# Performance work log

Hardware: AMD Instinct MI355X
Metric: run time of the kernel (lower is better)

The kernel has to match this reference:

```python
import jax, jax.numpy as jnp
import numpy as np
from jax import lax

B, T, L = 32, 64, 1500        # flows, max packets per flow, packet length (MTU)
H, DC = 128, 100              # lstm hidden, cnn feature dim
KS, ST = 5, 3                 # conv kernel/stride
FLAT = 54 * 32                # conv output length 1500->499->165->54, 32 channels


def setup_inputs() -> dict:
    key = jax.random.key(0)
    ks = jax.random.split(key, 12)
    s = 0.05
    X = jax.random.normal(ks[0], (B, T, L), jnp.float32)
    lengths = jax.random.randint(ks[1], (B,), 1, T + 1, dtype=jnp.int32)
    conv1_w = jax.random.normal(ks[2], (128, 1, KS), jnp.float32) * s
    conv2_w = jax.random.normal(ks[3], (32, 128, KS), jnp.float32) * s
    conv3_w = jax.random.normal(ks[4], (32, 32, KS), jnp.float32) * s
    lin_w = jax.random.normal(ks[5], (DC, FLAT), jnp.float32) * s
    w_ih0 = jax.random.normal(ks[6], (4 * H, DC), jnp.float32) * s
    w_hh0 = jax.random.normal(ks[7], (4 * H, H), jnp.float32) * s
    w_ih1 = jax.random.normal(ks[8], (4 * H, H), jnp.float32) * s
    w_hh1 = jax.random.normal(ks[9], (4 * H, H), jnp.float32) * s
    fc1_w = jax.random.normal(ks[10], (10, H), jnp.float32) * s
    fc2_w = jax.random.normal(ks[11], (2, 10), jnp.float32) * s
    return {"X": X, "lengths": lengths, "conv1_w": conv1_w, "conv2_w": conv2_w,
            "conv3_w": conv3_w, "lin_w": lin_w, "w_ih0": w_ih0, "w_hh0": w_hh0,
            "w_ih1": w_ih1, "w_hh1": w_hh1, "fc1_w": fc1_w, "fc2_w": fc2_w}


def _conv(x, w):
    # x: [N, Cin, L], w: [Cout, Cin, K] -> valid conv, stride 3 (torch Conv1d semantics)
    return lax.conv_general_dilated(x, w, (ST,), 'VALID',
                                    dimension_numbers=('NCH', 'OIH', 'NCH'))


def _lstm_layer(xs, mask, w_ih, w_hh):
    # xs: [T, B, D]; mask: [T, B] (True = valid step); no biases (bias=False)
    Bn = xs.shape[1]
    h0 = jnp.zeros((Bn, H), xs.dtype)
    c0 = jnp.zeros((Bn, H), xs.dtype)

    def step(carry, inp):
        h, c = carry
        x_t, m_t = inp
        gates = x_t @ w_ih.T + h @ w_hh.T          # [B, 4H]
        i, f, g, o = jnp.split(gates, 4, axis=-1)  # torch gate order i,f,g,o
        i, f, o = jax.nn.sigmoid(i), jax.nn.sigmoid(f), jax.nn.sigmoid(o)
        g = jnp.tanh(g)
        c_new = f * c + i * g
        h_new = o * jnp.tanh(c_new)
        m = m_t[:, None]
        h = jnp.where(m, h_new, h)  # freeze state past each flow's length
        c = jnp.where(m, c_new, c)
        return (h, c), h

    (h_f, c_f), hs = lax.scan(step, (h0, c0), (xs, mask))
    return hs, h_f


def reference(X, lengths, conv1_w, conv2_w, conv3_w, lin_w,
              w_ih0, w_hh0, w_ih1, w_hh1, fc1_w, fc2_w):
    leaky = jax.nn.leaky_relu  # slope 0.01 matches torch default
    # ODCNN over every packet (batched over all B*T packets instead of python loops)
    x = X.reshape(B * T, 1, L)
    x = leaky(_conv(x, conv1_w))   # [BT, 128, 499]
    x = leaky(_conv(x, conv2_w))   # [BT, 32, 165]
    x = leaky(_conv(x, conv3_w))   # [BT, 32, 54]
    feats = x.reshape(B * T, FLAT) @ lin_w.T          # [BT, 100] (no activation)
    feats = feats.reshape(B, T, DC).transpose(1, 0, 2)  # [T, B, 100]
    mask = jnp.arange(T)[:, None] < lengths[None, :]     # [T, B]
    hs1, _ = _lstm_layer(feats, mask, w_ih0, w_hh0)
    _, h2 = _lstm_layer(hs1, mask, w_ih1, w_hh1)         # h at step len-1, top layer
    out = leaky(h2 @ fc1_w.T)
    out = leaky(out @ fc2_w.T)                           # [B, out_dim]
    return out
```

## Files before the change

kernel.cpp:

```cpp
#include <hip/hip_runtime.h>
#include <hip/hip_bf16.h>

#define B_ 32
#define T_ 64
#define H_ 128
#define L3OUT 54
#define FLAT_ 1728

typedef __attribute__((ext_vector_type(8))) short bf16x8;
typedef __attribute__((ext_vector_type(4))) float f32x4;

__device__ __forceinline__ float leakyf(float v) { return v > 0.f ? v : 0.01f * v; }
__device__ __forceinline__ float sigmoidf_(float v) { return 1.f / (1.f + expf(-v)); }
__device__ __forceinline__ unsigned int bf16rne(float v) {
  unsigned int b = __float_as_uint(v);
  return (b + 0x7FFFu + ((b >> 16) & 1u)) >> 16;
}
__device__ __forceinline__ bf16x8 ldb8(const unsigned short* p) {
  return *(const bf16x8*)p;
}

__global__ __launch_bounds__(256) void k_prep(
    const float* __restrict__ w1, const float* __restrict__ w2,
    const float* __restrict__ w3, const float* __restrict__ linw,
    const float* __restrict__ wih0, const float* __restrict__ whh0,
    const float* __restrict__ wih1, const float* __restrict__ whh1,
    unsigned short* __restrict__ w1eh, unsigned short* __restrict__ w1el,
    unsigned short* __restrict__ w2h, unsigned short* __restrict__ w2l,
    unsigned short* __restrict__ w3h, unsigned short* __restrict__ w3l,
    unsigned short* __restrict__ linwh, unsigned short* __restrict__ linwl,
    unsigned short* __restrict__ wih0h, unsigned short* __restrict__ wih0l,
    float* __restrict__ whh0T, float* __restrict__ wih1T,
    float* __restrict__ whh1T) {
  const int e = blockIdx.x * 256 + threadIdx.x;
  if (e >= 264960) {
    int e5 = e - 264960;
    int m = e5 >> 16, r = e5 & 65535;
    int k = r >> 9, j = r & 511;
    const float* src = (m == 0) ? whh0 : ((m == 1) ? wih1 : whh1);
    float* dst = (m == 0) ? whh0T : ((m == 1) ? wih1T : whh1T);
    dst[r] = src[j * 128 + k];
    return;
  }
  float v;
  unsigned short* dh;
  unsigned short* dl;
  int di;
  if (e < 20480) {
    int cc = e / 5120, rem = e - cc * 5120;
    int c2 = rem / 160, r = rem - c2 * 160;
    int tap = r >> 5, c1l = r & 31;
    v = w2[c2 * 640 + (cc * 32 + c1l) * 5 + tap];
    dh = w2h; dl = w2l; di = e;
  } else if (e < 25600) {
    int e2 = e - 20480;
    int c3 = e2 / 160, r = e2 - c3 * 160;
    int tap = r >> 5, c2 = r & 31;
    v = w3[c3 * 160 + c2 * 5 + tap];
    dh = w3h; dl = w3l; di = e2;
  } else if (e < 198400) {
    int e3 = e - 25600;
    v = linw[e3];
    dh = linwh; dl = linwl; di = e3;
  } else if (e < 263936) {
    int e4 = e - 198400;
    int g = e4 >> 7, k = e4 & 127;
    v = (k < 100) ? wih0[g * 100 + k] : 0.f;
    dh = wih0h; dl = wih0l; di = e4;
  } else {
    int i = e - 263936;
    int c1 = i >> 3, j = i & 7;
    v = (j < 5) ? w1[c1 * 5 + j] : 0.f;
    dh = w1eh; dl = w1el; di = i;
  }
  unsigned int hb = bf16rne(v);
  float hf = __uint_as_float(hb << 16);
  unsigned int lb = bf16rne(v - hf);
  dh[di] = (unsigned short)hb;
  dl[di] = (unsigned short)lb;
}

__global__ __launch_bounds__(512) void k_conv123(
    const float* __restrict__ X, const float* __restrict__ w1,
    const unsigned short* __restrict__ w2h, const unsigned short* __restrict__ w2l,
    const unsigned short* __restrict__ w3h, const unsigned short* __restrict__ w3l,
    unsigned short* __restrict__ s3g) {
  __shared__ __align__(16) float Xs[1504];
  __shared__ __align__(16) unsigned int AhU[10640];

  const int n = blockIdx.x;
  const int tid = threadIdx.x;
  const int lane = tid & 63;
  const int w = tid >> 6;
  const int l15 = lane & 15;
  const int cg = lane >> 4;
  const int pr = tid & 15;
  const int po = tid >> 4;

  const float* Xn = X + (size_t)n * 1500;
  for (int i = tid; i < 1500; i += 512) Xs[i] = Xn[i];
  if (tid < 4) Xs[1500 + tid] = 0.f;
  for (int i = tid; i < 640; i += 512) AhU[10000 + i] = 0u;

  f32x4 acc2[2][2];
#pragma unroll
  for (int a = 0; a < 2; ++a)
#pragma unroll
    for (int m = 0; m < 2; ++m) acc2[a][m] = (f32x4){0.f, 0.f, 0.f, 0.f};

  for (int cc = 0; cc < 4; ++cc) {
    __syncthreads();
    const float* wA = w1 + (cc * 32 + 2 * pr) * 5;
    float a0 = wA[0], a1 = wA[1], a2 = wA[2], a3 = wA[3], a4 = wA[4];
    float b0 = wA[5], b1 = wA[6], b2 = wA[7], b3 = wA[8], b4 = wA[9];
#pragma unroll 2
    for (int i = 0; i < 16; ++i) {
      int pos = po + 32 * i;
      if (pos < 500) {
        const float* xp = Xs + 3 * pos;
        float x0 = xp[0], x1 = xp[1], x2 = xp[2], x3 = xp[3], x4 = xp[4];
        float vA = fmaf(x4, a4, fmaf(x3, a3, fmaf(x2, a2, fmaf(x1, a1, x0 * a0))));
        float vB = fmaf(x4, b4, fmaf(x3, b3, fmaf(x2, b2, fmaf(x1, b1, x0 * b0))));
        vA = leakyf(vA);
        vB = leakyf(vB);
        AhU[pos * 20 + pr] = bf16rne(vA) | (bf16rne(vB) << 16);
      }
    }
    __syncthreads();
    const unsigned short* w2hB = w2h + cc * 5120;
    const unsigned short* w2lB = w2l + cc * 5120;
#pragma unroll
    for (int tap = 0; tap < 5; ++tap) {
      const int wc = tap * 32 + cg * 8;
      bf16x8 ah0 = ldb8(w2hB + l15 * 160 + wc);
      bf16x8 ah1 = ldb8(w2hB + (l15 + 16) * 160 + wc);
      bf16x8 al0 = ldb8(w2lB + l15 * 160 + wc);
      bf16x8 al1 = ldb8(w2lB + (l15 + 16) * 160 + wc);
      {
        bf16x8 bfr = ldb8((const unsigned short*)AhU + (3 * (w * 16 + l15) + tap) * 40 + cg * 8);
        acc2[0][0] = __builtin_amdgcn_mfma_f32_16x16x32_bf16(ah0, bfr, acc2[0][0], 0, 0, 0);
        acc2[0][0] = __builtin_amdgcn_mfma_f32_16x16x32_bf16(al0, bfr, acc2[0][0], 0, 0, 0);
        acc2[0][1] = __builtin_amdgcn_mfma_f32_16x16x32_bf16(ah1, bfr, acc2[0][1], 0, 0, 0);
        acc2[0][1] = __builtin_amdgcn_mfma_f32_16x16x32_bf16(al1, bfr, acc2[0][1], 0, 0, 0);
      }
      if (w < 3) {
        int nt = 8 + w;
        bf16x8 bfr = ldb8((const unsigned short*)AhU + (3 * (nt * 16 + l15) + tap) * 40 + cg * 8);
        acc2[1][0] = __builtin_amdgcn_mfma_f32_16x16x32_bf16(ah0, bfr, acc2[1][0], 0, 0, 0);
        acc2[1][0] = __builtin_amdgcn_mfma_f32_16x16x32_bf16(al0, bfr, acc2[1][0], 0, 0, 0);
        acc2[1][1] = __builtin_amdgcn_mfma_f32_16x16x32_bf16(ah1, bfr, acc2[1][1], 0, 0, 0);
        acc2[1][1] = __builtin_amdgcn_mfma_f32_16x16x32_bf16(al1, bfr, acc2[1][1], 0, 0, 0);
      }
    }
  }
  __syncthreads();
  for (int i = tid; i < 400; i += 512) AhU[176 * 20 + i] = 0u;
#pragma unroll
  for (int nti = 0; nti < 2; ++nti) {
    int nt = (nti == 0) ? w : (8 + w);
    if (nti == 0 || w < 3) {
      int l2 = nt * 16 + l15;
#pragma unroll
      for (int mt = 0; mt < 2; ++mt) {
#pragma unroll
        for (int j = 0; j < 2; ++j) {
          float e0 = leakyf(acc2[nti][mt][2 * j]);
          float e1 = leakyf(acc2[nti][mt][2 * j + 1]);
          AhU[l2 * 20 + mt * 8 + cg * 2 + j] = bf16rne(e0) | (bf16rne(e1) << 16);
        }
      }
    }
  }
  __syncthreads();
  if (w < 4) {
    f32x4 a3[2];
    a3[0] = (f32x4){0.f, 0.f, 0.f, 0.f};
    a3[1] = (f32x4){0.f, 0.f, 0.f, 0.f};
#pragma unroll
    for (int tap = 0; tap < 5; ++tap) {
      const int wc = tap * 32 + cg * 8;
      bf16x8 wh0 = ldb8(w3h + l15 * 160 + wc);
      bf16x8 wh1 = ldb8(w3h + (l15 + 16) * 160 + wc);
      bf16x8 wl0 = ldb8(w3l + l15 * 160 + wc);
      bf16x8 wl1 = ldb8(w3l + (l15 + 16) * 160 + wc);
      bf16x8 bfr = ldb8((const unsigned short*)AhU + (3 * (w * 16 + l15) + tap) * 40 + cg * 8);
      a3[0] = __builtin_amdgcn_mfma_f32_16x16x32_bf16(wh0, bfr, a3[0], 0, 0, 0);
      a3[0] = __builtin_amdgcn_mfma_f32_16x16x32_bf16(wl0, bfr, a3[0], 0, 0, 0);
      a3[1] = __builtin_amdgcn_mfma_f32_16x16x32_bf16(wh1, bfr, a3[1], 0, 0, 0);
      a3[1] = __builtin_amdgcn_mfma_f32_16x16x32_bf16(wl1, bfr, a3[1], 0, 0, 0);
    }
    int l3 = w * 16 + l15;
    if (l3 < L3OUT) {
#pragma unroll
      for (int mt = 0; mt < 2; ++mt) {
#pragma unroll
        for (int r = 0; r < 4; ++r) {
          int c3 = mt * 16 + cg * 4 + r;
          s3g[(size_t)n * FLAT_ + c3 * L3OUT + l3] = (unsigned short)bf16rne(leakyf(a3[mt][r]));
        }
      }
    }
  }
}

__global__ __launch_bounds__(448) void k_gemm_fe(
    const unsigned short* __restrict__ s3g,
    const unsigned short* __restrict__ linwh, const unsigned short* __restrict__ linwl,
    unsigned short* __restrict__ feh, unsigned short* __restrict__ fel) {
  const int m0 = blockIdx.x * 16;
  const int tid = threadIdx.x;
  const int lane = tid & 63;
  const int w = tid >> 6;
  const int l15 = lane & 15;
  const int cg = lane >> 4;

  int brow = w * 16 + l15;
  if (brow > 99) brow = 99;
  const unsigned short* ap = s3g + (size_t)(m0 + l15) * FLAT_ + cg * 8;
  const unsigned short* bhp = linwh + (size_t)brow * FLAT_ + cg * 8;
  const unsigned short* blp = linwl + (size_t)brow * FLAT_ + cg * 8;

  f32x4 acc = (f32x4){0.f, 0.f, 0.f, 0.f};
#pragma unroll 6
  for (int ks = 0; ks < 54; ++ks) {
    bf16x8 af = ldb8(ap + ks * 32);
    bf16x8 bh = ldb8(bhp + ks * 32);
    bf16x8 bl = ldb8(blp + ks * 32);
    acc = __builtin_amdgcn_mfma_f32_16x16x32_bf16(af, bh, acc, 0, 0, 0);
    acc = __builtin_amdgcn_mfma_f32_16x16x32_bf16(af, bl, acc, 0, 0, 0);
  }
  const int jcol = w * 16 + l15;
  const int sample = m0 + cg * 4;
#pragma unroll
  for (int r = 0; r < 4; ++r) {
    float v = acc[r];
    unsigned int hb = bf16rne(v);
    float hf = __uint_as_float(hb << 16);
    unsigned int lb = bf16rne(v - hf);
    feh[(size_t)(sample + r) * 128 + jcol] = (unsigned short)hb;
    fel[(size_t)(sample + r) * 128 + jcol] = (unsigned short)lb;
  }
}

__global__ __launch_bounds__(256) void k_gemm_xg0(
    const unsigned short* __restrict__ feh, const unsigned short* __restrict__ fel,
    const unsigned short* __restrict__ wih0h, const unsigned short* __restrict__ wih0l,
    float* __restrict__ xg0) {
  const int m0 = blockIdx.x * 64;
  const int n0 = blockIdx.y * 128;
  const int tid = threadIdx.x;
  const int lane = tid & 63;
  const int w = tid >> 6;
  const int l15 = lane & 15;
  const int cg = lane >> 4;

  f32x4 acc[8];
#pragma unroll
  for (int i = 0; i < 8; ++i) acc[i] = (f32x4){0.f, 0.f, 0.f, 0.f};

  const int arow = m0 + w * 16 + l15;
#pragma unroll
  for (int ks = 0; ks < 4; ++ks) {
    bf16x8 ah = ldb8(feh + (size_t)arow * 128 + ks * 32 + cg * 8);
    bf16x8 al = ldb8(fel + (size_t)arow * 128 + ks * 32 + cg * 8);
#pragma unroll
    for (int nt = 0; nt < 8; ++nt) {
      int brow = n0 + nt * 16 + l15;
      bf16x8 bh = ldb8(wih0h + (size_t)brow * 128 + ks * 32 + cg * 8);
      bf16x8 bl = ldb8(wih0l + (size_t)brow * 128 + ks * 32 + cg * 8);
      acc[nt] = __builtin_amdgcn_mfma_f32_16x16x32_bf16(ah, bh, acc[nt], 0, 0, 0);
      acc[nt] = __builtin_amdgcn_mfma_f32_16x16x32_bf16(ah, bl, acc[nt], 0, 0, 0);
      acc[nt] = __builtin_amdgcn_mfma_f32_16x16x32_bf16(al, bh, acc[nt], 0, 0, 0);
    }
  }
#pragma unroll
  for (int nt = 0; nt < 8; ++nt) {
#pragma unroll
    for (int r = 0; r < 4; ++r) {
      xg0[(size_t)(m0 + w * 16 + cg * 4 + r) * 512 + n0 + nt * 16 + l15] = acc[nt][r];
    }
  }
}

__global__ __launch_bounds__(512) void k_lstm0(
    const float* __restrict__ xg0, const float* __restrict__ whh0T,
    const int* __restrict__ lengths, float* __restrict__ hs1) {
  __shared__ __align__(16) float h0s[H_];
  __shared__ float ps[16 * 128];
  const int b = blockIdx.x;
  const int tid = threadIdx.x;
  const int ks = tid >> 7;
  const int jj = tid & 127;
  float w[4][32];
#pragma unroll
  for (int kk = 0; kk < 32; ++kk) {
#pragma unroll
    for (int q = 0; q < 4; ++q)
      w[q][kk] = whh0T[(ks * 32 + kk) * 512 + q * 128 + jj];
  }
  if (tid < H_) h0s[tid] = 0.f;
  float c = 0.f;
  const int len = lengths[b];
  float xq0 = 0.f, xq1 = 0.f, xq2 = 0.f, xq3 = 0.f;
  if (tid < H_) {
    const float* xp = xg0 + (size_t)(b * T_) * 512;
    xq0 = xp[jj]; xq1 = xp[128 + jj]; xq2 = xp[256 + jj]; xq3 = xp[384 + jj];
  }
  __syncthreads();
  for (int t = 0; t < len; ++t) {
    float p0 = 0.f, p1 = 0.f, p2 = 0.f, p3 = 0.f;
#pragma unroll
    for (int k4 = 0; k4 < 8; ++k4) {
      float4 hv = *(const float4*)(h0s + ks * 32 + k4 * 4);
      p0 = fmaf(hv.x, w[0][k4 * 4], fmaf(hv.y, w[0][k4 * 4 + 1], fmaf(hv.z, w[0][k4 * 4 + 2], fmaf(hv.w, w[0][k4 * 4 + 3], p0))));
      p1 = fmaf(hv.x, w[1][k4 * 4], fmaf(hv.y, w[1][k4 * 4 + 1], fmaf(hv.z, w[1][k4 * 4 + 2], fmaf(hv.w, w[1][k4 * 4 + 3], p1))));
      p2 = fmaf(hv.x, w[2][k4 * 4], fmaf(hv.y, w[2][k4 * 4 + 1], fmaf(hv.z, w[2][k4 * 4 + 2], fmaf(hv.w, w[2][k4 * 4 + 3], p2))));
      p3 = fmaf(hv.x, w[3][k4 * 4], fmaf(hv.y, w[3][k4 * 4 + 1], fmaf(hv.z, w[3][k4 * 4 + 2], fmaf(hv.w, w[3][k4 * 4 + 3], p3))));
    }
    ps[(ks * 4 + 0) * 128 + jj] = p0;
    ps[(ks * 4 + 1) * 128 + jj] = p1;
    ps[(ks * 4 + 2) * 128 + jj] = p2;
    ps[(ks * 4 + 3) * 128 + jj] = p3;
    __syncthreads();
    if (tid < H_) {
      float gi = xq0 + ((ps[0 * 128 + jj] + ps[4 * 128 + jj]) + (ps[8 * 128 + jj] + ps[12 * 128 + jj]));
      float gf = xq1 + ((ps[1 * 128 + jj] + ps[5 * 128 + jj]) + (ps[9 * 128 + jj] + ps[13 * 128 + jj]));
      float gg = xq2 + ((ps[2 * 128 + jj] + ps[6 * 128 + jj]) + (ps[10 * 128 + jj] + ps[14 * 128 + jj]));
      float go = xq3 + ((ps[3 * 128 + jj] + ps[7 * 128 + jj]) + (ps[11 * 128 + jj] + ps[15 * 128 + jj]));
      float ig = sigmoidf_(gi);
      float fg = sigmoidf_(gf);
      float gt = tanhf(gg);
      float og = sigmoidf_(go);
      c = fg * c + ig * gt;
      float hn = og * tanhf(c);
      h0s[jj] = hn;
      hs1[((size_t)(b * T_ + t)) * H_ + jj] = hn;
      if (t + 1 < len) {
        const float* xp = xg0 + (size_t)(b * T_ + t + 1) * 512;
        xq0 = xp[jj]; xq1 = xp[128 + jj]; xq2 = xp[256 + jj]; xq3 = xp[384 + jj];
      }
    }
    __syncthreads();
  }
}

__global__ __launch_bounds__(512) void k_xg1(
    const float* __restrict__ hs1, const float* __restrict__ wih1T,
    float* __restrict__ xg1) {
  __shared__ __align__(16) float hsS[8][128];
  const int r0 = blockIdx.x * 8;
  const int tid = threadIdx.x;
  for (int i = tid; i < 8 * 128; i += 512) ((float*)hsS)[i] = hs1[(size_t)r0 * 128 + i];
  __syncthreads();
  float acc[8] = {0.f, 0.f, 0.f, 0.f, 0.f, 0.f, 0.f, 0.f};
#pragma unroll 4
  for (int k4 = 0; k4 < 32; ++k4) {
    float w0 = wih1T[(4 * k4 + 0) * 512 + tid];
    float w1v = wih1T[(4 * k4 + 1) * 512 + tid];
    float w2v = wih1T[(4 * k4 + 2) * 512 + tid];
    float w3v = wih1T[(4 * k4 + 3) * 512 + tid];
#pragma unroll
    for (int i = 0; i < 8; ++i) {
      float4 h = *(const float4*)(&hsS[i][4 * k4]);
      acc[i] += h.x * w0 + h.y * w1v + h.z * w2v + h.w * w3v;
    }
  }
#pragma unroll
  for (int i = 0; i < 8; ++i) xg1[((size_t)(r0 + i)) * 512 + tid] = acc[i];
}

__global__ __launch_bounds__(512) void k_lstm1(
    const float* __restrict__ xg1, const float* __restrict__ whh1T,
    const float* __restrict__ fc1, const float* __restrict__ fc2,
    const int* __restrict__ lengths, float* __restrict__ out) {
  __shared__ __align__(16) float h1s[H_];
  __shared__ float ps[16 * 128];
  __shared__ float tmp10[10];
  const int b = blockIdx.x;
  const int tid = threadIdx.x;
  const int ks = tid >> 7;
  const int jj = tid & 127;
  float w[4][32];
#pragma unroll
  for (int kk = 0; kk < 32; ++kk) {
#pragma unroll
    for (int q = 0; q < 4; ++q)
      w[q][kk] = whh1T[(ks * 32 + kk) * 512 + q * 128 + jj];
  }
  if (tid < H_) h1s[tid] = 0.f;
  float c = 0.f;
  const int len = lengths[b];
  float xq0 = 0.f, xq1 = 0.f, xq2 = 0.f, xq3 = 0.f;
  if (tid < H_) {
    const float* xp = xg1 + (size_t)(b * T_) * 512;
    xq0 = xp[jj]; xq1 = xp[128 + jj]; xq2 = xp[256 + jj]; xq3 = xp[384 + jj];
  }
  __syncthreads();
  for (int t = 0; t < len; ++t) {
    float p0 = 0.f, p1 = 0.f, p2 = 0.f, p3 = 0.f;
#pragma unroll
    for (int k4 = 0; k4 < 8; ++k4) {
      float4 hv = *(const float4*)(h1s + ks * 32 + k4 * 4);
      p0 = fmaf(hv.x, w[0][k4 * 4], fmaf(hv.y, w[0][k4 * 4 + 1], fmaf(hv.z, w[0][k4 * 4 + 2], fmaf(hv.w, w[0][k4 * 4 + 3], p0))));
      p1 = fmaf(hv.x, w[1][k4 * 4], fmaf(hv.y, w[1][k4 * 4 + 1], fmaf(hv.z, w[1][k4 * 4 + 2], fmaf(hv.w, w[1][k4 * 4 + 3], p1))));
      p2 = fmaf(hv.x, w[2][k4 * 4], fmaf(hv.y, w[2][k4 * 4 + 1], fmaf(hv.z, w[2][k4 * 4 + 2], fmaf(hv.w, w[2][k4 * 4 + 3], p2))));
      p3 = fmaf(hv.x, w[3][k4 * 4], fmaf(hv.y, w[3][k4 * 4 + 1], fmaf(hv.z, w[3][k4 * 4 + 2], fmaf(hv.w, w[3][k4 * 4 + 3], p3))));
    }
    ps[(ks * 4 + 0) * 128 + jj] = p0;
    ps[(ks * 4 + 1) * 128 + jj] = p1;
    ps[(ks * 4 + 2) * 128 + jj] = p2;
    ps[(ks * 4 + 3) * 128 + jj] = p3;
    __syncthreads();
    if (tid < H_) {
      float gi = xq0 + ((ps[0 * 128 + jj] + ps[4 * 128 + jj]) + (ps[8 * 128 + jj] + ps[12 * 128 + jj]));
      float gf = xq1 + ((ps[1 * 128 + jj] + ps[5 * 128 + jj]) + (ps[9 * 128 + jj] + ps[13 * 128 + jj]));
      float gg = xq2 + ((ps[2 * 128 + jj] + ps[6 * 128 + jj]) + (ps[10 * 128 + jj] + ps[14 * 128 + jj]));
      float go = xq3 + ((ps[3 * 128 + jj] + ps[7 * 128 + jj]) + (ps[11 * 128 + jj] + ps[15 * 128 + jj]));
      float ig = sigmoidf_(gi);
      float fg = sigmoidf_(gf);
      float gt = tanhf(gg);
      float og = sigmoidf_(go);
      c = fg * c + ig * gt;
      float hn = og * tanhf(c);
      h1s[jj] = hn;
      if (t + 1 < len) {
        const float* xp = xg1 + (size_t)(b * T_ + t + 1) * 512;
        xq0 = xp[jj]; xq1 = xp[128 + jj]; xq2 = xp[256 + jj]; xq3 = xp[384 + jj];
      }
    }
    __syncthreads();
  }
  if (tid < 10) {
    const float* fr = fc1 + tid * H_;
    float s = 0.f;
#pragma unroll 4
    for (int k = 0; k < H_; ++k) s += h1s[k] * fr[k];
    tmp10[tid] = leakyf(s);
  }
  __syncthreads();
  if (tid < 2) {
    const float* fr = fc2 + tid * 10;
    float s = 0.f;
#pragma unroll
    for (int j = 0; j < 10; ++j) s += tmp10[j] * fr[j];
    out[b * 2 + tid] = leakyf(s);
  }
}

extern "C" void kernel_launch(void* const* d_in, const int* in_sizes, int n_in,
                              void* d_out, int out_size, void* d_ws, size_t ws_size,
                              hipStream_t stream) {
  const float* X = (const float*)d_in[0];
  const int* lengths = (const int*)d_in[1];
  const float* w1 = (const float*)d_in[2];
  const float* w2 = (const float*)d_in[3];
  const float* w3 = (const float*)d_in[4];
  const float* linw = (const float*)d_in[5];
  const float* wih0 = (const float*)d_in[6];
  const float* whh0 = (const float*)d_in[7];
  const float* wih1 = (const float*)d_in[8];
  const float* whh1 = (const float*)d_in[9];
  const float* fc1 = (const float*)d_in[10];
  const float* fc2 = (const float*)d_in[11];

  char* wsb = (char*)d_ws;
  size_t off = 0;
  auto alloc = [&](size_t bytes) {
    char* p = wsb + off;
    off += (bytes + 511) & ~(size_t)511;
    return p;
  };
  unsigned short* s3g = (unsigned short*)alloc(2048 * 1728 * 2);
  unsigned short* feh = (unsigned short*)alloc(2048 * 128 * 2);
  unsigned short* fel = (unsigned short*)alloc(2048 * 128 * 2);
  float* xg0 = (float*)alloc(2048 * 512 * 4);
  unsigned short* w1eh = (unsigned short*)alloc(1024 * 2);
  unsigned short* w1el = (unsigned short*)alloc(1024 * 2);
  unsigned short* w2h = (unsigned short*)alloc(20480 * 2);
  unsigned short* w2l = (unsigned short*)alloc(20480 * 2);
  unsigned short* w3h = (unsigned short*)alloc(5120 * 2);
  unsigned short* w3l = (unsigned short*)alloc(5120 * 2);
  unsigned short* linwh = (unsigned short*)alloc(172800 * 2);
  unsigned short* linwl = (unsigned short*)alloc(172800 * 2);
  unsigned short* wih0h = (unsigned short*)alloc(65536 * 2);
  unsigned short* wih0l = (unsigned short*)alloc(65536 * 2);
  float* whh0T = (float*)alloc(65536 * 4);
  float* wih1T = (float*)alloc(65536 * 4);
  float* whh1T = (float*)alloc(65536 * 4);
  float* hs1 = (float*)alloc(262144 * 4);
  float* xg1 = (float*)alloc(2048 * 512 * 4);

  k_prep<<<1803, 256, 0, stream>>>(w1, w2, w3, linw, wih0, whh0, wih1, whh1,
                                   w1eh, w1el, w2h, w2l, w3h, w3l,
                                   linwh, linwl, wih0h, wih0l,
                                   whh0T, wih1T, whh1T);
  k_conv123<<<2048, 512, 0, stream>>>(X, w1, w2h, w2l, w3h, w3l, s3g);
  k_gemm_fe<<<128, 448, 0, stream>>>(s3g, linwh, linwl, feh, fel);
  k_gemm_xg0<<<dim3(32, 4), 256, 0, stream>>>(feh, fel, wih0h, wih0l, xg0);
  k_lstm0<<<32, 512, 0, stream>>>(xg0, whh0T, lengths, hs1);
  k_xg1<<<256, 512, 0, stream>>>(hs1, wih1T, xg1);
  k_lstm1<<<32, 512, 0, stream>>>(xg1, whh1T, fc1, fc2, lengths, (float*)d_out);
}
```

Baseline: 296.8 us.

## Fuse feature GEMM with input-gate GEMM and restructure conv1 thread mapping

The linear-feature GEMM and the layer-0 input-gate GEMM are merged into one kernel. The 16x100 feature tile stays in shared memory as a bf16 hi/lo pair and is multiplied by W_ih0 directly, which removes one launch and the feh/fel round trip through global memory. Separately, conv1 now gives each thread one output position: its five input samples are loaded into registers once, it computes all 32 channels of a chunk, and it writes them with vectorized shared stores. In exchange, the fused kernel runs on only 128 blocks for the gate GEMM, and conv1 reads its weights from global memory in every thread.

```diff
diff --git a/kernel.cpp b/kernel.cpp
--- a/kernel.cpp
+++ b/kernel.cpp
@@ -94,13 +94,18 @@
   const int w = tid >> 6;
   const int l15 = lane & 15;
   const int cg = lane >> 4;
-  const int pr = tid & 15;
-  const int po = tid >> 4;
 
   const float* Xn = X + (size_t)n * 1500;
   for (int i = tid; i < 1500; i += 512) Xs[i] = Xn[i];
   if (tid < 4) Xs[1500 + tid] = 0.f;
   for (int i = tid; i < 640; i += 512) AhU[10000 + i] = 0u;
+  __syncthreads();
+
+  float x0 = 0.f, x1 = 0.f, x2 = 0.f, x3 = 0.f, x4 = 0.f;
+  if (tid < 500) {
+    const float* xp = Xs + 3 * tid;
+    x0 = xp[0]; x1 = xp[1]; x2 = xp[2]; x3 = xp[3]; x4 = xp[4];
+  }
 
   f32x4 acc2[2][2];
 #pragma unroll
@@ -110,21 +115,21 @@
 
   for (int cc = 0; cc < 4; ++cc) {
     __syncthreads();
-    const float* wA = w1 + (cc * 32 + 2 * pr) * 5;
-    float a0 = wA[0], a1 = wA[1], a2 = wA[2], a3 = wA[3], a4 = wA[4];
-    float b0 = wA[5], b1 = wA[6], b2 = wA[7], b3 = wA[8], b4 = wA[9];
-#pragma unroll 2
-    for (int i = 0; i < 16; ++i) {
-      int pos = po + 32 * i;
-      if (pos < 500) {
-        const float* xp = Xs + 3 * pos;
-        float x0 = xp[0], x1 = xp[1], x2 = xp[2], x3 = xp[3], x4 = xp[4];
-        float vA = fmaf(x4, a4, fmaf(x3, a3, fmaf(x2, a2, fmaf(x1, a1, x0 * a0))));
-        float vB = fmaf(x4, b4, fmaf(x3, b3, fmaf(x2, b2, fmaf(x1, b1, x0 * b0))));
-        vA = leakyf(vA);
-        vB = leakyf(vB);
-        AhU[pos * 20 + pr] = bf16rne(vA) | (bf16rne(vB) << 16);
-      }
+    if (tid < 500) {
+      const float* wc = w1 + cc * 160;
+      unsigned int rowbuf[16];
+#pragma unroll
+      for (int p = 0; p < 16; ++p) {
+        const float* wa = wc + 10 * p;
+        float vA = fmaf(x4, wa[4], fmaf(x3, wa[3], fmaf(x2, wa[2], fmaf(x1, wa[1], x0 * wa[0]))));
+        float vB = fmaf(x4, wa[9], fmaf(x3, wa[8], fmaf(x2, wa[7], fmaf(x1, wa[6], x0 * wa[5]))));
+        vA = fmaxf(vA, 0.01f * vA);
+        vB = fmaxf(vB, 0.01f * vB);
+        rowbuf[p] = bf16rne(vA) | (bf16rne(vB) << 16);
+      }
+#pragma unroll
+      for (int q = 0; q < 4; ++q)
+        *(uint4*)(&AhU[tid * 20 + 4 * q]) = *(uint4*)(&rowbuf[4 * q]);
     }
     __syncthreads();
     const unsigned short* w2hB = w2h + cc * 5120;
@@ -203,16 +208,26 @@
   }
 }
 
-__global__ __launch_bounds__(448) void k_gemm_fe(
+__global__ __launch_bounds__(448) void k_gemm_fx(
     const unsigned short* __restrict__ s3g,
     const unsigned short* __restrict__ linwh, const unsigned short* __restrict__ linwl,
-    unsigned short* __restrict__ feh, unsigned short* __restrict__ fel) {
+    const unsigned short* __restrict__ wih0h, const unsigned short* __restrict__ wih0l,
+    float* __restrict__ xg0) {
+  __shared__ __align__(16) unsigned short fehS[16][136];
+  __shared__ __align__(16) unsigned short felS[16][136];
+
   const int m0 = blockIdx.x * 16;
   const int tid = threadIdx.x;
   const int lane = tid & 63;
   const int w = tid >> 6;
   const int l15 = lane & 15;
   const int cg = lane >> 4;
+
+  if (tid < 192) {
+    int r = tid / 12, c = tid - r * 12;
+    ((unsigned int*)&fehS[r][112])[c] = 0u;
+    ((unsigned int*)&felS[r][112])[c] = 0u;
+  }
 
   int brow = w * 16 + l15;
   if (brow > 99) brow = 99;
@@ -230,54 +245,36 @@
     acc = __builtin_amdgcn_mfma_f32_16x16x32_bf16(af, bl, acc, 0, 0, 0);
   }
   const int jcol = w * 16 + l15;
-  const int sample = m0 + cg * 4;
 #pragma unroll
   for (int r = 0; r < 4; ++r) {
     float v = acc[r];
     unsigned int hb = bf16rne(v);
     float hf = __uint_as_float(hb << 16);
     unsigned int lb = bf16rne(v - hf);
-    feh[(size_t)(sample + r) * 128 + jcol] = (unsigned short)hb;
-    fel[(size_t)(sample + r) * 128 + jcol] = (unsigned short)lb;
-  }
-}
-
-__global__ __launch_bounds__(256) void k_gemm_xg0(
-    const unsigned short* __restrict__ feh, const unsigned short* __restrict__ fel,
-    const unsigned short* __restrict__ wih0h, const unsigned short* __restrict__ wih0l,
-    float* __restrict__ xg0) {
-  const int m0 = blockIdx.x * 64;
-  const int n0 = blockIdx.y * 128;
-  const int tid = threadIdx.x;
-  const int lane = tid & 63;
-  const int w = tid >> 6;
-  const int l15 = lane & 15;
-  const int cg = lane >> 4;
-
-  f32x4 acc[8];
-#pragma unroll
-  for (int i = 0; i < 8; ++i) acc[i] = (f32x4){0.f, 0.f, 0.f, 0.f};
-
-  const int arow = m0 + w * 16 + l15;
-#pragma unroll
-  for (int ks = 0; ks < 4; ++ks) {
-    bf16x8 ah = ldb8(feh + (size_t)arow * 128 + ks * 32 + cg * 8);
-    bf16x8 al = ldb8(fel + (size_t)arow * 128 + ks * 32 + cg * 8);
-#pragma unroll
-    for (int nt = 0; nt < 8; ++nt) {
-      int brow = n0 + nt * 16 + l15;
-      bf16x8 bh = ldb8(wih0h + (size_t)brow * 128 + ks * 32 + cg * 8);
-      bf16x8 bl = ldb8(wih0l + (size_t)brow * 128 + ks * 32 + cg * 8);
-      acc[nt] = __builtin_amdgcn_mfma_f32_16x16x32_bf16(ah, bh, acc[nt], 0, 0, 0);
-      acc[nt] = __builtin_amdgcn_mfma_f32_16x16x32_bf16(ah, bl, acc[nt], 0, 0, 0);
-      acc[nt] = __builtin_amdgcn_mfma_f32_16x16x32_bf16(al, bh, acc[nt], 0, 0, 0);
-    }
-  }
-#pragma unroll
-  for (int nt = 0; nt < 8; ++nt) {
-#pragma unroll
-    for (int r = 0; r < 4; ++r) {
-      xg0[(size_t)(m0 + w * 16 + cg * 4 + r) * 512 + n0 + nt * 16 + l15] = acc[nt][r];
+    fehS[cg * 4 + r][jcol] = (unsigned short)hb;
+    felS[cg * 4 + r][jcol] = (unsigned short)lb;
+  }
+  __syncthreads();
+
+#pragma unroll
+  for (int nt0 = 0; nt0 < 5; ++nt0) {
+    int nt = w + 7 * nt0;
+    if (nt < 32) {
+      f32x4 a = (f32x4){0.f, 0.f, 0.f, 0.f};
+#pragma unroll
+      for (int ks = 0; ks < 4; ++ks) {
+        bf16x8 ah = ldb8(&fehS[l15][ks * 32 + cg * 8]);
+        bf16x8 al = ldb8(&felS[l15][ks * 32 + cg * 8]);
+        int br = nt * 16 + l15;
+        bf16x8 bh = ldb8(wih0h + (size_t)br * 128 + ks * 32 + cg * 8);
+        bf16x8 bl = ldb8(wih0l + (size_t)br * 128 + ks * 32 + cg * 8);
+        a = __builtin_amdgcn_mfma_f32_16x16x32_bf16(ah, bh, a, 0, 0, 0);
+        a = __builtin_amdgcn_mfma_f32_16x16x32_bf16(ah, bl, a, 0, 0, 0);
+        a = __builtin_amdgcn_mfma_f32_16x16x32_bf16(al, bh, a, 0, 0, 0);
+      }
+#pragma unroll
+      for (int r = 0; r < 4; ++r)
+        xg0[(size_t)(m0 + cg * 4 + r) * 512 + nt * 16 + l15] = a[r];
     }
   }
 }
@@ -471,8 +468,6 @@
     return p;
   };
   unsigned short* s3g = (unsigned short*)alloc(2048 * 1728 * 2);
-  unsigned short* feh = (unsigned short*)alloc(2048 * 128 * 2);
-  unsigned short* fel = (unsigned short*)alloc(2048 * 128 * 2);
   float* xg0 = (float*)alloc(2048 * 512 * 4);
   unsigned short* w1eh = (unsigned short*)alloc(1024 * 2);
   unsigned short* w1el = (unsigned short*)alloc(1024 * 2);
@@ -495,8 +490,7 @@
                                    linwh, linwl, wih0h, wih0l,
                                    whh0T, wih1T, whh1T);
   k_conv123<<<2048, 512, 0, stream>>>(X, w1, w2h, w2l, w3h, w3l, s3g);
-  k_gemm_fe<<<128, 448, 0, stream>>>(s3g, linwh, linwl, feh, fel);
-  k_gemm_xg0<<<dim3(32, 4), 256, 0, stream>>>(feh, fel, wih0h, wih0l, xg0);
+  k_gemm_fx<<<128, 448, 0, stream>>>(s3g, linwh, linwl, wih0h, wih0l, xg0);
   k_lstm0<<<32, 512, 0, stream>>>(xg0, whh0T, lengths, hs1);
   k_xg1<<<256, 512, 0, stream>>>(hs1, wih1T, xg1);
   k_lstm1<<<32, 512, 0, stream>>>(xg1, whh1T, fc1, fc2, lengths, (float*)d_out);
```

New measurement: 284.2 us. -4.3%, faster.
